# Performance work log

Measured on AMD Instinct MI355X. Metric: run time of the kernel, lower is better.

The kernel has to match this reference:

```python
import jax, jax.numpy as jnp
import numpy as np

EPS = 1e-8  # torch.nn.functional.cosine_similarity default eps


def setup_inputs() -> dict:
    key = jax.random.key(0)
    k1, k2 = jax.random.split(key)
    P, B, D = 64, 512, 1024
    z_list = jax.random.normal(k1, (P, B, D), dtype=jnp.float32)
    z_avg = jax.random.normal(k2, (B, D), dtype=jnp.float32)  # passed but unused (overwritten in forward)
    return {"z_list": z_list, "z_avg": z_avg}


def reference(z_list, z_avg):
    # z_list: (P, B, D). The original overwrites z_avg with the patch mean.
    P, B, _ = z_list.shape
    z_avg = jnp.mean(z_list, axis=0)  # (B, D)

    # cosine_similarity(z_list[p,i], z_avg[j]) via normalize + batched matmul
    zn = z_list / jnp.maximum(jnp.linalg.norm(z_list, axis=-1, keepdims=True), EPS)
    an = z_avg / jnp.maximum(jnp.linalg.norm(z_avg, axis=-1, keepdims=True), EPS)
    cos_sim = jnp.einsum("pbd,cd->pbc", zn, an) - 1.0  # (P, B, B)

    mask = ~jnp.eye(B, dtype=bool)  # zero out diagonal (i == j)
    z_dissim = jnp.sum(cos_sim * mask[None, :, :])
    count = jnp.sum(mask) * P  # B*(B-1)*P
    return z_dissim / count
```

## Files before the change

kernel.cpp:

```cpp
#include <hip/hip_runtime.h>
#include <math.h>

constexpr int P = 64, B = 512, D = 1024;
constexpr int D4 = D / 4;
constexpr int WAVES = 4;
constexpr int PC = P / WAVES;
constexpr int K3B = 32;
constexpr int BPB = B / K3B;
#define EPS 1e-8f

__device__ inline float wave_reduce_sum(float v) {
#pragma unroll
  for (int off = 1; off < 64; off <<= 1) v += __shfl_xor(v, off);
  return v;
}

__device__ inline float dot4(const float4& a, const float4& b) {
  return a.x * b.x + a.y * b.y + a.z * b.z + a.w * b.w;
}

__global__ __launch_bounds__(256) void k_main(const float* __restrict__ z,
                                              float* __restrict__ an,
                                              float* __restrict__ Uv,
                                              float* __restrict__ diag) {
  const int b = blockIdx.x;
  const int t = threadIdx.x;
  const int w = t >> 6;
  const int lane = t & 63;

  __shared__ float4 lds_zs[WAVES][D4];
  __shared__ float4 lds_uu[WAVES][D4];
  __shared__ float red[2 * WAVES];

  float4 zs[4], uu[4];
#pragma unroll
  for (int k = 0; k < 4; ++k) {
    zs[k] = make_float4(0.f, 0.f, 0.f, 0.f);
    uu[k] = make_float4(0.f, 0.f, 0.f, 0.f);
  }

  const size_t pstride = (size_t)B * D4;
  const float4* base = (const float4*)z + ((size_t)(w * PC) * B + b) * D4;

  float4 curA[4], curB[4];
#pragma unroll
  for (int k = 0; k < 4; ++k) {
    curA[k] = base[k * 64 + lane];
    curB[k] = base[pstride + k * 64 + lane];
  }

  for (int pr = 0; pr < PC / 2; ++pr) {
    float4 nxtA[4], nxtB[4];
    const bool more = (pr + 1 < PC / 2);
    if (more) {
      const float4* nA = base + (size_t)(2 * pr + 2) * pstride;
      const float4* nB = base + (size_t)(2 * pr + 3) * pstride;
#pragma unroll
      for (int k = 0; k < 4; ++k) {
        nxtA[k] = nA[k * 64 + lane];
        nxtB[k] = nB[k * 64 + lane];
      }
    }

    float ssA = 0.f, ssB = 0.f;
#pragma unroll
    for (int k = 0; k < 4; ++k) {
      ssA += dot4(curA[k], curA[k]);
      ssB += dot4(curB[k], curB[k]);
    }
#pragma unroll
    for (int off = 1; off < 64; off <<= 1) {
      ssA += __shfl_xor(ssA, off);
      ssB += __shfl_xor(ssB, off);
    }
    const float wA = 1.0f / fmaxf(sqrtf(ssA), EPS);
    const float wB = 1.0f / fmaxf(sqrtf(ssB), EPS);

#pragma unroll
    for (int k = 0; k < 4; ++k) {
      zs[k].x += curA[k].x + curB[k].x;
      zs[k].y += curA[k].y + curB[k].y;
      zs[k].z += curA[k].z + curB[k].z;
      zs[k].w += curA[k].w + curB[k].w;
      uu[k].x += wA * curA[k].x + wB * curB[k].x;
      uu[k].y += wA * curA[k].y + wB * curB[k].y;
      uu[k].z += wA * curA[k].z + wB * curB[k].z;
      uu[k].w += wA * curA[k].w + wB * curB[k].w;
    }
    if (more) {
#pragma unroll
      for (int k = 0; k < 4; ++k) {
        curA[k] = nxtA[k];
        curB[k] = nxtB[k];
      }
    }
  }

#pragma unroll
  for (int k = 0; k < 4; ++k) {
    lds_zs[w][k * 64 + lane] = zs[k];
    lds_uu[w][k * 64 + lane] = uu[k];
  }
  __syncthreads();

  float4 zsum = make_float4(0.f, 0.f, 0.f, 0.f);
  float4 usum = make_float4(0.f, 0.f, 0.f, 0.f);
#pragma unroll
  for (int ww = 0; ww < WAVES; ++ww) {
    float4 a = lds_zs[ww][t];
    float4 u = lds_uu[ww][t];
    zsum.x += a.x; zsum.y += a.y; zsum.z += a.z; zsum.w += a.w;
    usum.x += u.x; usum.y += u.y; usum.z += u.z; usum.w += u.w;
  }

  float ss = dot4(zsum, zsum);
  ss = wave_reduce_sum(ss);
  if (lane == 0) red[w] = ss;
  __syncthreads();
  ss = red[0] + red[1] + red[2] + red[3];

  const float inv = 1.0f / fmaxf(sqrtf(ss), (float)P * EPS);
  float4 a4 = make_float4(zsum.x * inv, zsum.y * inv, zsum.z * inv, zsum.w * inv);

  ((float4*)an)[(size_t)b * D4 + t] = a4;
  ((float4*)Uv)[(size_t)b * D4 + t] = usum;

  float dg = dot4(usum, a4);
  dg = wave_reduce_sum(dg);
  if (lane == 0) red[WAVES + w] = dg;
  __syncthreads();
  if (t == 0) diag[b] = red[WAVES] + red[WAVES + 1] + red[WAVES + 2] + red[WAVES + 3];
}

__global__ __launch_bounds__(256) void k3_colsum(const float* __restrict__ an,
                                                 const float* __restrict__ Uv,
                                                 float* __restrict__ Spart,
                                                 float* __restrict__ Tpart) {
  const int blk = blockIdx.x;
  const int t = threadIdx.x;
  float4 s = make_float4(0.f, 0.f, 0.f, 0.f);
  float4 tt = make_float4(0.f, 0.f, 0.f, 0.f);
#pragma unroll 4
  for (int i = 0; i < BPB; ++i) {
    const size_t b = (size_t)blk * BPB + i;
    float4 a = ((const float4*)an)[b * D4 + t];
    float4 u = ((const float4*)Uv)[b * D4 + t];
    s.x += a.x; s.y += a.y; s.z += a.z; s.w += a.w;
    tt.x += u.x; tt.y += u.y; tt.z += u.z; tt.w += u.w;
  }
  ((float4*)Spart)[(size_t)blk * D4 + t] = s;
  ((float4*)Tpart)[(size_t)blk * D4 + t] = tt;
}

__global__ __launch_bounds__(256) void k4_final(const float* __restrict__ Spart,
                                                const float* __restrict__ Tpart,
                                                const float* __restrict__ diag,
                                                float* __restrict__ out) {
  const int t = threadIdx.x;
  __shared__ float red[4];
  float4 S = make_float4(0.f, 0.f, 0.f, 0.f);
  float4 T = make_float4(0.f, 0.f, 0.f, 0.f);
#pragma unroll 4
  for (int blk = 0; blk < K3B; ++blk) {
    float4 s = ((const float4*)Spart)[(size_t)blk * D4 + t];
    float4 u = ((const float4*)Tpart)[(size_t)blk * D4 + t];
    S.x += s.x; S.y += s.y; S.z += s.z; S.w += s.w;
    T.x += u.x; T.y += u.y; T.z += u.z; T.w += u.w;
  }
  float local = dot4(S, T) - diag[t] - diag[t + 256];
  local = wave_reduce_sum(local);
  const int wid = t >> 6;
  if ((t & 63) == 0) red[wid] = local;
  __syncthreads();
  if (t == 0) {
    const float tot = red[0] + red[1] + red[2] + red[3];
    const float count = 64.0f * 512.0f * 511.0f;
    out[0] = tot / count - 1.0f;
  }
}

extern "C" void kernel_launch(void* const* d_in, const int* in_sizes, int n_in,
                              void* d_out, int out_size, void* d_ws, size_t ws_size,
                              hipStream_t stream) {
  const float* z = (const float*)d_in[0];

  float* ws = (float*)d_ws;
  float* an = ws;
  float* Uv = an + (size_t)B * D;
  float* diag = Uv + (size_t)B * D;
  float* Spart = diag + B;
  float* Tpart = Spart + (size_t)K3B * D;

  k_main<<<B, 256, 0, stream>>>(z, an, Uv, diag);
  k3_colsum<<<K3B, 256, 0, stream>>>(an, Uv, Spart, Tpart);
  k4_final<<<1, 256, 0, stream>>>(Spart, Tpart, diag, (float*)d_out);
}
```

Measured before the change: 35.22 us.

## Fuse column-sum and final reduction into main kernel via atomics and last-block

Replaces the three-kernel pipeline with one kernel. Each block atomically adds its normalized mean and weighted-sum vectors into global accumulators, plus its diagonal term, and the last block (found with an atomic counter) computes the final dot product. This removes the intermediate B×D writes and reads and two kernel launches. In exchange it adds a memset, heavy float atomic contention on 2048 addresses from 512 blocks, and a nondeterministic summation order.

After: 104.1 us. +195.6%, slower.

```diff
diff --git a/kernel.cpp b/kernel.cpp
--- a/kernel.cpp
+++ b/kernel.cpp
@@ -5,8 +5,6 @@
 constexpr int D4 = D / 4;
 constexpr int WAVES = 4;
 constexpr int PC = P / WAVES;
-constexpr int K3B = 32;
-constexpr int BPB = B / K3B;
 #define EPS 1e-8f
 
 __device__ inline float wave_reduce_sum(float v) {
@@ -19,10 +17,12 @@
   return a.x * b.x + a.y * b.y + a.z * b.z + a.w * b.w;
 }
 
-__global__ __launch_bounds__(256) void k_main(const float* __restrict__ z,
-                                              float* __restrict__ an,
-                                              float* __restrict__ Uv,
-                                              float* __restrict__ diag) {
+__global__ __launch_bounds__(256) void k_fused(const float* __restrict__ z,
+                                               float* __restrict__ Sfin,
+                                               float* __restrict__ Tfin,
+                                               float* __restrict__ diagsum,
+                                               int* __restrict__ counter,
+                                               float* __restrict__ out) {
   const int b = blockIdx.x;
   const int t = threadIdx.x;
   const int w = t >> 6;
@@ -122,60 +122,51 @@
   const float inv = 1.0f / fmaxf(sqrtf(ss), (float)P * EPS);
   float4 a4 = make_float4(zsum.x * inv, zsum.y * inv, zsum.z * inv, zsum.w * inv);
 
-  ((float4*)an)[(size_t)b * D4 + t] = a4;
-  ((float4*)Uv)[(size_t)b * D4 + t] = usum;
+  atomicAdd(&Sfin[4 * t + 0], a4.x);
+  atomicAdd(&Sfin[4 * t + 1], a4.y);
+  atomicAdd(&Sfin[4 * t + 2], a4.z);
+  atomicAdd(&Sfin[4 * t + 3], a4.w);
+  atomicAdd(&Tfin[4 * t + 0], usum.x);
+  atomicAdd(&Tfin[4 * t + 1], usum.y);
+  atomicAdd(&Tfin[4 * t + 2], usum.z);
+  atomicAdd(&Tfin[4 * t + 3], usum.w);
 
   float dg = dot4(usum, a4);
   dg = wave_reduce_sum(dg);
   if (lane == 0) red[WAVES + w] = dg;
   __syncthreads();
-  if (t == 0) diag[b] = red[WAVES] + red[WAVES + 1] + red[WAVES + 2] + red[WAVES + 3];
-}
+  if (t == 0) {
+    const float dtot = red[WAVES] + red[WAVES + 1] + red[WAVES + 2] + red[WAVES + 3];
+    atomicAdd(diagsum, dtot);
+  }
 
-__global__ __launch_bounds__(256) void k3_colsum(const float* __restrict__ an,
-                                                 const float* __restrict__ Uv,
-                                                 float* __restrict__ Spart,
-                                                 float* __restrict__ Tpart) {
-  const int blk = blockIdx.x;
-  const int t = threadIdx.x;
-  float4 s = make_float4(0.f, 0.f, 0.f, 0.f);
-  float4 tt = make_float4(0.f, 0.f, 0.f, 0.f);
-#pragma unroll 4
-  for (int i = 0; i < BPB; ++i) {
-    const size_t b = (size_t)blk * BPB + i;
-    float4 a = ((const float4*)an)[b * D4 + t];
-    float4 u = ((const float4*)Uv)[b * D4 + t];
-    s.x += a.x; s.y += a.y; s.z += a.z; s.w += a.w;
-    tt.x += u.x; tt.y += u.y; tt.z += u.z; tt.w += u.w;
+  __threadfence();
+  __syncthreads();
+  __shared__ int is_last;
+  if (t == 0) {
+    int old = atomicAdd(counter, 1);
+    is_last = (old == B - 1);
   }
-  ((float4*)Spart)[(size_t)blk * D4 + t] = s;
-  ((float4*)Tpart)[(size_t)blk * D4 + t] = tt;
-}
+  __syncthreads();
+  if (!is_last) return;
 
-__global__ __launch_bounds__(256) void k4_final(const float* __restrict__ Spart,
-                                                const float* __restrict__ Tpart,
-                                                const float* __restrict__ diag,
-                                                float* __restrict__ out) {
-  const int t = threadIdx.x;
-  __shared__ float red[4];
-  float4 S = make_float4(0.f, 0.f, 0.f, 0.f);
-  float4 T = make_float4(0.f, 0.f, 0.f, 0.f);
-#pragma unroll 4
-  for (int blk = 0; blk < K3B; ++blk) {
-    float4 s = ((const float4*)Spart)[(size_t)blk * D4 + t];
-    float4 u = ((const float4*)Tpart)[(size_t)blk * D4 + t];
-    S.x += s.x; S.y += s.y; S.z += s.z; S.w += s.w;
-    T.x += u.x; T.y += u.y; T.z += u.z; T.w += u.w;
+  __threadfence();
+  float local = 0.f;
+#pragma unroll
+  for (int k = 0; k < 4; ++k) {
+    float sv = __hip_atomic_load(&Sfin[4 * t + k], __ATOMIC_RELAXED, __HIP_MEMORY_SCOPE_AGENT);
+    float tv = __hip_atomic_load(&Tfin[4 * t + k], __ATOMIC_RELAXED, __HIP_MEMORY_SCOPE_AGENT);
+    local += sv * tv;
   }
-  float local = dot4(S, T) - diag[t] - diag[t + 256];
   local = wave_reduce_sum(local);
-  const int wid = t >> 6;
-  if ((t & 63) == 0) red[wid] = local;
+  __shared__ float red2[4];
+  if (lane == 0) red2[w] = local;
   __syncthreads();
   if (t == 0) {
-    const float tot = red[0] + red[1] + red[2] + red[3];
+    const float dot = red2[0] + red2[1] + red2[2] + red2[3];
+    const float dsum = __hip_atomic_load(diagsum, __ATOMIC_RELAXED, __HIP_MEMORY_SCOPE_AGENT);
     const float count = 64.0f * 512.0f * 511.0f;
-    out[0] = tot / count - 1.0f;
+    out[0] = (dot - dsum) / count - 1.0f;
   }
 }
 
@@ -185,13 +176,11 @@
   const float* z = (const float*)d_in[0];
 
   float* ws = (float*)d_ws;
-  float* an = ws;
-  float* Uv = an + (size_t)B * D;
-  float* diag = Uv + (size_t)B * D;
-  float* Spart = diag + B;
-  float* Tpart = Spart + (size_t)K3B * D;
+  float* Sfin = ws;
+  float* Tfin = Sfin + D;
+  float* diagsum = Tfin + D;
+  int* counter = (int*)(diagsum + 1);
 
-  k_main<<<B, 256, 0, stream>>>(z, an, Uv, diag);
-  k3_colsum<<<K3B, 256, 0, stream>>>(an, Uv, Spart, Tpart);
-  k4_final<<<1, 256, 0, stream>>>(Spart, Tpart, diag, (float*)d_out);
+  hipMemsetAsync(d_ws, 0, (2 * D + 2) * sizeof(float), stream);
+  k_fused<<<B, 256, 0, stream>>>(z, Sfin, Tfin, diagsum, counter, (float*)d_out);
 }
```

## Merge column-sum and final reduction into one tail kernel with atomics

Applied to the files above, without the earlier changes.

Replaces the two-kernel tail (row-block column sums, then a single-block final reduction) with one kernel. Each of its 32 blocks owns a slice of 32 feature columns, reduces all rows for them, computes its slice of the dot product plus part of the diagonal correction, and atomically adds its contribution to the output. The output is zeroed inside the main kernel. This removes one launch and the partial-sum round trip through global memory, at the cost of a float atomic whose ordering makes the result order-dependent.

New measurement: 31.97 us. 1.1x faster.

```diff
diff --git a/kernel.cpp b/kernel.cpp
--- a/kernel.cpp
+++ b/kernel.cpp
@@ -5,8 +5,7 @@
 constexpr int D4 = D / 4;
 constexpr int WAVES = 4;
 constexpr int PC = P / WAVES;
-constexpr int K3B = 32;
-constexpr int BPB = B / K3B;
+constexpr int TB = 32;
 #define EPS 1e-8f
 
 __device__ inline float wave_reduce_sum(float v) {
@@ -22,11 +21,14 @@
 __global__ __launch_bounds__(256) void k_main(const float* __restrict__ z,
                                               float* __restrict__ an,
                                               float* __restrict__ Uv,
-                                              float* __restrict__ diag) {
+                                              float* __restrict__ diag,
+                                              float* __restrict__ out) {
   const int b = blockIdx.x;
   const int t = threadIdx.x;
   const int w = t >> 6;
   const int lane = t & 63;
+
+  if (b == 0 && t == 0) out[0] = 0.f;
 
   __shared__ float4 lds_zs[WAVES][D4];
   __shared__ float4 lds_uu[WAVES][D4];
@@ -132,50 +134,66 @@
   if (t == 0) diag[b] = red[WAVES] + red[WAVES + 1] + red[WAVES + 2] + red[WAVES + 3];
 }
 
-__global__ __launch_bounds__(256) void k3_colsum(const float* __restrict__ an,
-                                                 const float* __restrict__ Uv,
-                                                 float* __restrict__ Spart,
-                                                 float* __restrict__ Tpart) {
+__global__ __launch_bounds__(256) void k_tail(const float* __restrict__ an,
+                                              const float* __restrict__ Uv,
+                                              const float* __restrict__ diag,
+                                              float* __restrict__ out) {
   const int blk = blockIdx.x;
   const int t = threadIdx.x;
-  float4 s = make_float4(0.f, 0.f, 0.f, 0.f);
-  float4 tt = make_float4(0.f, 0.f, 0.f, 0.f);
-#pragma unroll 4
-  for (int i = 0; i < BPB; ++i) {
-    const size_t b = (size_t)blk * BPB + i;
-    float4 a = ((const float4*)an)[b * D4 + t];
-    float4 u = ((const float4*)Uv)[b * D4 + t];
-    s.x += a.x; s.y += a.y; s.z += a.z; s.w += a.w;
-    tt.x += u.x; tt.y += u.y; tt.z += u.z; tt.w += u.w;
-  }
-  ((float4*)Spart)[(size_t)blk * D4 + t] = s;
-  ((float4*)Tpart)[(size_t)blk * D4 + t] = tt;
-}
-
-__global__ __launch_bounds__(256) void k4_final(const float* __restrict__ Spart,
-                                                const float* __restrict__ Tpart,
-                                                const float* __restrict__ diag,
-                                                float* __restrict__ out) {
-  const int t = threadIdx.x;
-  __shared__ float red[4];
+  const int w = t >> 6;
+  const int lane = t & 63;
+  const int f4c = blk * 8 + (t & 7);
+  const int rg = t >> 3;
+
   float4 S = make_float4(0.f, 0.f, 0.f, 0.f);
   float4 T = make_float4(0.f, 0.f, 0.f, 0.f);
 #pragma unroll 4
-  for (int blk = 0; blk < K3B; ++blk) {
-    float4 s = ((const float4*)Spart)[(size_t)blk * D4 + t];
-    float4 u = ((const float4*)Tpart)[(size_t)blk * D4 + t];
-    S.x += s.x; S.y += s.y; S.z += s.z; S.w += s.w;
+  for (int i = 0; i < 16; ++i) {
+    const size_t r = (size_t)rg + 32 * i;
+    float4 a = ((const float4*)an)[r * D4 + f4c];
+    float4 u = ((const float4*)Uv)[r * D4 + f4c];
+    S.x += a.x; S.y += a.y; S.z += a.z; S.w += a.w;
     T.x += u.x; T.y += u.y; T.z += u.z; T.w += u.w;
   }
-  float local = dot4(S, T) - diag[t] - diag[t + 256];
-  local = wave_reduce_sum(local);
-  const int wid = t >> 6;
-  if ((t & 63) == 0) red[wid] = local;
-  __syncthreads();
-  if (t == 0) {
-    const float tot = red[0] + red[1] + red[2] + red[3];
-    const float count = 64.0f * 512.0f * 511.0f;
-    out[0] = tot / count - 1.0f;
+
+#pragma unroll
+  for (int off = 8; off < 64; off <<= 1) {
+    S.x += __shfl_xor(S.x, off); S.y += __shfl_xor(S.y, off);
+    S.z += __shfl_xor(S.z, off); S.w += __shfl_xor(S.w, off);
+    T.x += __shfl_xor(T.x, off); T.y += __shfl_xor(T.y, off);
+    T.z += __shfl_xor(T.z, off); T.w += __shfl_xor(T.w, off);
+  }
+
+  __shared__ float4 ldsS[4][8], ldsT[4][8];
+  if (lane < 8) {
+    ldsS[w][lane] = S;
+    ldsT[w][lane] = T;
+  }
+  __syncthreads();
+
+  float dotp = 0.f;
+  if (t < 8) {
+    float4 Sf = ldsS[0][t], Tf = ldsT[0][t];
+#pragma unroll
+    for (int ww = 1; ww < 4; ++ww) {
+      float4 s2 = ldsS[ww][t], t2 = ldsT[ww][t];
+      Sf.x += s2.x; Sf.y += s2.y; Sf.z += s2.z; Sf.w += s2.w;
+      Tf.x += t2.x; Tf.y += t2.y; Tf.z += t2.z; Tf.w += t2.w;
+    }
+    dotp = dot4(Sf, Tf);
+  }
+  float dgp = 0.f;
+  if (t >= 16 && t < 32) dgp = diag[blk * 16 + (t - 16)];
+
+  if (w == 0) {
+    float v = dotp - dgp;
+#pragma unroll
+    for (int off = 1; off < 32; off <<= 1) v += __shfl_xor(v, off);
+    if (t == 0) {
+      const float count = 64.0f * 512.0f * 511.0f;
+      float contrib = v / count + (blk == 0 ? -1.0f : 0.0f);
+      atomicAdd(out, contrib);
+    }
   }
 }
 
@@ -188,10 +206,7 @@
   float* an = ws;
   float* Uv = an + (size_t)B * D;
   float* diag = Uv + (size_t)B * D;
-  float* Spart = diag + B;
-  float* Tpart = Spart + (size_t)K3B * D;
-
-  k_main<<<B, 256, 0, stream>>>(z, an, Uv, diag);
-  k3_colsum<<<K3B, 256, 0, stream>>>(an, Uv, Spart, Tpart);
-  k4_final<<<1, 256, 0, stream>>>(Spart, Tpart, diag, (float*)d_out);
-}
+
+  k_main<<<B, 256, 0, stream>>>(z, an, Uv, diag, (float*)d_out);
+  k_tail<<<TB, 256, 0, stream>>>(an, Uv, diag, (float*)d_out);
+}
```
